# Optimization experiments

Hardware: AMD Instinct MI355X
Metric: run time of the kernel (lower is better)

## Reference

```python
import jax, jax.numpy as jnp
import numpy as np

C_IN = 256
A = 2086
H_BOARD, W_BOARD = 10, 9
S = H_BOARD * W_BOARD  # 90
E = 2                  # embed dim after 1x1 conv
NH = 2                 # num attention heads (head_dim = 1)
B = 4096
BN_EPS = 1e-5


def setup_inputs() -> dict:
    key = jax.random.key(0)
    ks = jax.random.split(key, 12)
    inp = {
        "x": jax.random.normal(ks[0], (B, C_IN, H_BOARD, W_BOARD), dtype=jnp.float32),
        # 1x1 conv, no bias: weight [out=2, in=256]
        "conv_w": jax.random.normal(ks[1], (E, C_IN), dtype=jnp.float32) * 0.05,
        # BatchNorm2d(2) params / running stats (inference-mode BN)
        "bn_gamma": jnp.ones((E,), dtype=jnp.float32),
        "bn_beta": jnp.zeros((E,), dtype=jnp.float32),
        "bn_mean": jax.random.normal(ks[2], (E,), dtype=jnp.float32) * 0.1,
        "bn_var": jax.random.uniform(ks[3], (E,), dtype=jnp.float32, minval=0.5, maxval=1.5),
        # MultiheadAttention packed in-proj: [3*E, E], bias [3*E]
        "in_proj_w": jax.random.normal(ks[4], (3 * E, E), dtype=jnp.float32) * 0.5,
        "in_proj_b": jax.random.normal(ks[5], (3 * E,), dtype=jnp.float32) * 0.05,
        "out_proj_w": jax.random.normal(ks[6], (E, E), dtype=jnp.float32) * 0.5,
        "out_proj_b": jax.random.normal(ks[7], (E,), dtype=jnp.float32) * 0.05,
        # Linear(2*90 -> 2086)
        "fc_w": jax.random.normal(ks[8], (A, E * S), dtype=jnp.float32) * 0.05,
        "fc_b": jax.random.normal(ks[9], (A,), dtype=jnp.float32) * 0.05,
    }
    return inp


def reference(x, conv_w, bn_gamma, bn_beta, bn_mean, bn_var,
              in_proj_w, in_proj_b, out_proj_w, out_proj_b, fc_w, fc_b):
    b = x.shape[0]
    # 1x1 conv (bias-free) == channel contraction: [b,256,h,w] -> [b,2,h,w]
    y = jnp.einsum('bchw,oc->bohw', x, conv_w)
    # BatchNorm2d (inference): (y - mean) / sqrt(var + eps) * gamma + beta
    scale = (bn_gamma * jax.lax.rsqrt(bn_var + BN_EPS))[None, :, None, None]
    shift = (bn_beta - bn_mean * bn_gamma * jax.lax.rsqrt(bn_var + BN_EPS))[None, :, None, None]
    y = y * scale + shift
    # [b,2,h,w] -> [b, S, 2]  (seq = board cells, feature = 2 channels)
    xf = y.reshape(b, E, S).transpose(0, 2, 1)
    # packed QKV projection
    qkv = xf @ in_proj_w.T + in_proj_b          # [b,S,3E]
    q, k, v = jnp.split(qkv, 3, axis=-1)        # each [b,S,E]
    hd = E // NH                                 # head_dim = 1
    def split_heads(t):
        return t.reshape(b, S, NH, hd).transpose(0, 2, 1, 3)  # [b,nh,S,hd]
    q, k, v = split_heads(q), split_heads(k), split_heads(v)
    scores = jnp.einsum('bhqd,bhkd->bhqk', q, k) / jnp.sqrt(jnp.float32(hd))
    attn = jax.nn.softmax(scores, axis=-1)      # [b,nh,S,S]
    o = jnp.einsum('bhqk,bhkd->bhqd', attn, v)  # [b,nh,S,hd]
    o = o.transpose(0, 2, 1, 3).reshape(b, S, E)
    o = o @ out_proj_w.T + out_proj_b           # [b,S,E]
    # [b,S,E] -> [b,E,S] -> [b, E*S], matching permute(0,2,1).view(b,-1)
    flat = o.transpose(0, 2, 1).reshape(b, E * S)
    logits = flat @ fc_w.T + fc_b               # [b, 2086]
    return logits
```

## Files before the change

### kernel.cpp

```cpp
#include <hip/hip_runtime.h>

#define C_IN    256
#define S_CELLS 90
#define A_OUT   2086
#define K_FC    180
#define B_BATCH 4096

__global__ __launch_bounds__(384) void front_kernel(
    const float* __restrict__ x,
    const float* __restrict__ conv_w,
    const float* __restrict__ bn_gamma,
    const float* __restrict__ bn_beta,
    const float* __restrict__ bn_mean,
    const float* __restrict__ bn_var,
    const float* __restrict__ ipw,
    const float* __restrict__ ipb,
    const float* __restrict__ opw,
    const float* __restrict__ opb,
    float* __restrict__ flat)
{
    __shared__ float4 kvpack[4][S_CELLS];

    const int sub = threadIdx.x / 96;
    const int s   = threadIdx.x % 96;
    const int b   = blockIdx.x * 4 + sub;

    float q0 = 0.f, q1 = 0.f;

    if (s < S_CELLS) {
        const float* xb = x + (size_t)b * (C_IN * S_CELLS) + s;
        float a0 = 0.f, a1 = 0.f;
        #pragma unroll 16
        for (int c = 0; c < C_IN; ++c) {
            float xv = xb[(size_t)c * S_CELLS];
            a0 = fmaf(conv_w[c], xv, a0);
            a1 = fmaf(conv_w[C_IN + c], xv, a1);
        }
        const float sc0 = bn_gamma[0] * rsqrtf(bn_var[0] + 1e-5f);
        const float sc1 = bn_gamma[1] * rsqrtf(bn_var[1] + 1e-5f);
        const float y0 = a0 * sc0 + (bn_beta[0] - bn_mean[0] * sc0);
        const float y1 = a1 * sc1 + (bn_beta[1] - bn_mean[1] * sc1);
        q0 = ipw[0] * y0 + ipw[1] * y1 + ipb[0];
        q1 = ipw[2] * y0 + ipw[3] * y1 + ipb[1];
        const float k0 = ipw[4] * y0 + ipw[5]  * y1 + ipb[2];
        const float k1 = ipw[6] * y0 + ipw[7]  * y1 + ipb[3];
        const float v0 = ipw[8] * y0 + ipw[9]  * y1 + ipb[4];
        const float v1 = ipw[10]* y0 + ipw[11] * y1 + ipb[5];
        kvpack[sub][s] = make_float4(k0, v0, k1, v1);
    }
    __syncthreads();
    if (s < S_CELLS) {
        float den0 = 0.f, num0 = 0.f, den1 = 0.f, num1 = 0.f;
        #pragma unroll 5
        for (int j = 0; j < S_CELLS; ++j) {
            const float4 kv = kvpack[sub][j];
            const float e0 = __expf(q0 * kv.x);
            const float e1 = __expf(q1 * kv.z);
            den0 += e0; num0 = fmaf(e0, kv.y, num0);
            den1 += e1; num1 = fmaf(e1, kv.w, num1);
        }
        const float o0 = num0 / den0;
        const float o1 = num1 / den1;
        const float r0 = opw[0] * o0 + opw[1] * o1 + opb[0];
        const float r1 = opw[2] * o0 + opw[3] * o1 + opb[1];
        flat[(size_t)b * K_FC + s]           = r0;
        flat[(size_t)b * K_FC + S_CELLS + s] = r1;
    }
}

#define BM 128
#define BN 128
#define BK 36
#define KV4 (BK / 4)

__global__ __launch_bounds__(256) void fc_kernel(
    const float* __restrict__ Af,
    const float* __restrict__ W,
    const float* __restrict__ bias,
    float* __restrict__ out)
{
    __shared__ __align__(16) float As[BK][BM + 4];
    __shared__ __align__(16) float Bs[BK][BN + 4];

    const int tid = threadIdx.x;
    const int tx  = tid & 15;
    const int ty  = tid >> 4;
    const int bm  = blockIdx.y * BM;
    const int bn  = blockIdx.x * BN;

    float acc[8][8] = {};

    for (int k0 = 0; k0 < K_FC; k0 += BK) {
        for (int q = tid; q < BM * KV4; q += 256) {
            const int m  = q / KV4;
            const int kv = q % KV4;
            const float4 v = *(const float4*)(Af + (size_t)(bm + m) * K_FC + k0 + kv * 4);
            const int kk = kv * 4;
            As[kk + 0][m] = v.x; As[kk + 1][m] = v.y;
            As[kk + 2][m] = v.z; As[kk + 3][m] = v.w;
        }
        for (int q = tid; q < BN * KV4; q += 256) {
            const int n  = q / KV4;
            const int kv = q % KV4;
            const int gn = bn + n;
            float4 v = make_float4(0.f, 0.f, 0.f, 0.f);
            if (gn < A_OUT)
                v = *(const float4*)(W + (size_t)gn * K_FC + k0 + kv * 4);
            const int kk = kv * 4;
            Bs[kk + 0][n] = v.x; Bs[kk + 1][n] = v.y;
            Bs[kk + 2][n] = v.z; Bs[kk + 3][n] = v.w;
        }
        __syncthreads();

        #pragma unroll 4
        for (int k = 0; k < BK; ++k) {
            float a[8], bb[8];
            const float4 a0 = *(const float4*)&As[k][ty * 8];
            const float4 a1 = *(const float4*)&As[k][ty * 8 + 4];
            const float4 b0 = *(const float4*)&Bs[k][tx * 8];
            const float4 b1 = *(const float4*)&Bs[k][tx * 8 + 4];
            a[0]=a0.x; a[1]=a0.y; a[2]=a0.z; a[3]=a0.w;
            a[4]=a1.x; a[5]=a1.y; a[6]=a1.z; a[7]=a1.w;
            bb[0]=b0.x; bb[1]=b0.y; bb[2]=b0.z; bb[3]=b0.w;
            bb[4]=b1.x; bb[5]=b1.y; bb[6]=b1.z; bb[7]=b1.w;
            #pragma unroll
            for (int i = 0; i < 8; ++i)
                #pragma unroll
                for (int j = 0; j < 8; ++j)
                    acc[i][j] = fmaf(a[i], bb[j], acc[i][j]);
        }
        __syncthreads();
    }

    #pragma unroll
    for (int i = 0; i < 8; ++i) {
        const int gm = bm + ty * 8 + i;
        #pragma unroll
        for (int p = 0; p < 4; ++p) {
            const int gn = bn + tx * 8 + p * 2;
            if (gn < A_OUT) {
                float2 v = make_float2(acc[i][p * 2]     + bias[gn],
                                       acc[i][p * 2 + 1] + bias[gn + 1]);
                *(float2*)(out + (size_t)gm * A_OUT + gn) = v;
            }
        }
    }
}

extern "C" void kernel_launch(void* const* d_in, const int* in_sizes, int n_in,
                              void* d_out, int out_size, void* d_ws, size_t ws_size,
                              hipStream_t stream) {
    const float* x        = (const float*)d_in[0];
    const float* conv_w   = (const float*)d_in[1];
    const float* bn_gamma = (const float*)d_in[2];
    const float* bn_beta  = (const float*)d_in[3];
    const float* bn_mean  = (const float*)d_in[4];
    const float* bn_var   = (const float*)d_in[5];
    const float* ipw      = (const float*)d_in[6];
    const float* ipb      = (const float*)d_in[7];
    const float* opw      = (const float*)d_in[8];
    const float* opb      = (const float*)d_in[9];
    const float* fc_w     = (const float*)d_in[10];
    const float* fc_b     = (const float*)d_in[11];
    float* out  = (float*)d_out;
    float* flat = (float*)d_ws;

    front_kernel<<<dim3(B_BATCH / 4), 384, 0, stream>>>(
        x, conv_w, bn_gamma, bn_beta, bn_mean, bn_var,
        ipw, ipb, opw, opb, flat);

    fc_kernel<<<dim3((A_OUT + BN - 1) / BN, B_BATCH / BM), 256, 0, stream>>>(
        flat, fc_w, fc_b, out);
}
```

Measured before the change: 593.7 us.

## Run FC layer on bf16 MFMA with padded bf16 activations and weights

The front kernel now writes its activations as bf16, zero-padded to K=192. A new kernel converts fc_w to padded bf16 on every call. The fp32 FMA GEMM is replaced with a bf16 MFMA 16x16x32 kernel that loads 64-wide K tiles into LDS. This moves the GEMM onto matrix cores and halves operand bytes, at the cost of bf16 precision loss and an extra weight-conversion launch.

```diff
diff --git a/kernel.cpp b/kernel.cpp
--- a/kernel.cpp
+++ b/kernel.cpp
@@ -4,7 +4,17 @@
 #define S_CELLS 90
 #define A_OUT   2086
 #define K_FC    180
+#define K_PAD   192
+#define N_PAD   2176
 #define B_BATCH 4096
+
+typedef __attribute__((ext_vector_type(8))) short short8;
+typedef __attribute__((ext_vector_type(4))) float floatx4;
+
+static __device__ __forceinline__ unsigned short f2bf(float f) {
+    unsigned u = __float_as_uint(f);
+    return (unsigned short)((u + 0x7FFFu + ((u >> 16) & 1u)) >> 16);
+}
 
 __global__ __launch_bounds__(384) void front_kernel(
     const float* __restrict__ x,
@@ -17,7 +27,7 @@
     const float* __restrict__ ipb,
     const float* __restrict__ opw,
     const float* __restrict__ opb,
-    float* __restrict__ flat)
+    unsigned short* __restrict__ Abf)
 {
     __shared__ float4 kvpack[4][S_CELLS];
 
@@ -63,86 +73,91 @@
         const float o1 = num1 / den1;
         const float r0 = opw[0] * o0 + opw[1] * o1 + opb[0];
         const float r1 = opw[2] * o0 + opw[3] * o1 + opb[1];
-        flat[(size_t)b * K_FC + s]           = r0;
-        flat[(size_t)b * K_FC + S_CELLS + s] = r1;
+        Abf[(size_t)b * K_PAD + s]           = f2bf(r0);
+        Abf[(size_t)b * K_PAD + S_CELLS + s] = f2bf(r1);
+    } else {
+        Abf[(size_t)b * K_PAD + 180 + (s - S_CELLS)] = 0;
+        Abf[(size_t)b * K_PAD + 186 + (s - S_CELLS)] = 0;
     }
+}
+
+__global__ __launch_bounds__(192) void wconv_kernel(
+    const float* __restrict__ W, unsigned short* __restrict__ Wbf)
+{
+    const int n = blockIdx.x;
+    const int k = threadIdx.x;
+    unsigned short v = 0;
+    if (n < A_OUT && k < K_FC) v = f2bf(W[(size_t)n * K_FC + k]);
+    Wbf[(size_t)n * K_PAD + k] = v;
 }
 
 #define BM 128
 #define BN 128
-#define BK 36
-#define KV4 (BK / 4)
+#define BK 64
+#define LDSROW 72
 
-__global__ __launch_bounds__(256) void fc_kernel(
-    const float* __restrict__ Af,
-    const float* __restrict__ W,
+__global__ __launch_bounds__(256) void fc_mfma_kernel(
+    const unsigned short* __restrict__ Abf,
+    const unsigned short* __restrict__ Wbf,
     const float* __restrict__ bias,
     float* __restrict__ out)
 {
-    __shared__ __align__(16) float As[BK][BM + 4];
-    __shared__ __align__(16) float Bs[BK][BN + 4];
+    __shared__ __align__(16) unsigned short As[BM * LDSROW];
+    __shared__ __align__(16) unsigned short Bs[BN * LDSROW];
 
-    const int tid = threadIdx.x;
-    const int tx  = tid & 15;
-    const int ty  = tid >> 4;
-    const int bm  = blockIdx.y * BM;
-    const int bn  = blockIdx.x * BN;
+    const int tid  = threadIdx.x;
+    const int lane = tid & 63;
+    const int wave = tid >> 6;
+    const int wy   = wave >> 1;
+    const int wx   = wave & 1;
+    const int lrow = lane & 15;
+    const int lk   = (lane >> 4) * 8;
+    const int bm   = blockIdx.y * BM;
+    const int bn   = blockIdx.x * BN;
 
-    float acc[8][8] = {};
+    floatx4 acc[4][4] = {};
 
-    for (int k0 = 0; k0 < K_FC; k0 += BK) {
-        for (int q = tid; q < BM * KV4; q += 256) {
-            const int m  = q / KV4;
-            const int kv = q % KV4;
-            const float4 v = *(const float4*)(Af + (size_t)(bm + m) * K_FC + k0 + kv * 4);
-            const int kk = kv * 4;
-            As[kk + 0][m] = v.x; As[kk + 1][m] = v.y;
-            As[kk + 2][m] = v.z; As[kk + 3][m] = v.w;
-        }
-        for (int q = tid; q < BN * KV4; q += 256) {
-            const int n  = q / KV4;
-            const int kv = q % KV4;
-            const int gn = bn + n;
-            float4 v = make_float4(0.f, 0.f, 0.f, 0.f);
-            if (gn < A_OUT)
-                v = *(const float4*)(W + (size_t)gn * K_FC + k0 + kv * 4);
-            const int kk = kv * 4;
-            Bs[kk + 0][n] = v.x; Bs[kk + 1][n] = v.y;
-            Bs[kk + 2][n] = v.z; Bs[kk + 3][n] = v.w;
+    for (int k0 = 0; k0 < K_PAD; k0 += BK) {
+        for (int q = tid; q < BM * 8; q += 256) {
+            const int m = q >> 3, c = q & 7;
+            *(int4*)&As[m * LDSROW + c * 8] =
+                *(const int4*)(Abf + (size_t)(bm + m) * K_PAD + k0 + c * 8);
+            *(int4*)&Bs[m * LDSROW + c * 8] =
+                *(const int4*)(Wbf + (size_t)(bn + m) * K_PAD + k0 + c * 8);
         }
         __syncthreads();
 
-        #pragma unroll 4
-        for (int k = 0; k < BK; ++k) {
-            float a[8], bb[8];
-            const float4 a0 = *(const float4*)&As[k][ty * 8];
-            const float4 a1 = *(const float4*)&As[k][ty * 8 + 4];
-            const float4 b0 = *(const float4*)&Bs[k][tx * 8];
-            const float4 b1 = *(const float4*)&Bs[k][tx * 8 + 4];
-            a[0]=a0.x; a[1]=a0.y; a[2]=a0.z; a[3]=a0.w;
-            a[4]=a1.x; a[5]=a1.y; a[6]=a1.z; a[7]=a1.w;
-            bb[0]=b0.x; bb[1]=b0.y; bb[2]=b0.z; bb[3]=b0.w;
-            bb[4]=b1.x; bb[5]=b1.y; bb[6]=b1.z; bb[7]=b1.w;
+        #pragma unroll
+        for (int ks = 0; ks < 2; ++ks) {
+            short8 af[4], bf[4];
             #pragma unroll
-            for (int i = 0; i < 8; ++i)
+            for (int t = 0; t < 4; ++t) {
+                af[t] = *(const short8*)&As[(wy * 64 + t * 16 + lrow) * LDSROW + ks * 32 + lk];
+                bf[t] = *(const short8*)&Bs[(wx * 64 + t * 16 + lrow) * LDSROW + ks * 32 + lk];
+            }
+            #pragma unroll
+            for (int mt = 0; mt < 4; ++mt)
                 #pragma unroll
-                for (int j = 0; j < 8; ++j)
-                    acc[i][j] = fmaf(a[i], bb[j], acc[i][j]);
+                for (int nt = 0; nt < 4; ++nt)
+                    acc[mt][nt] = __builtin_amdgcn_mfma_f32_16x16x32_bf16(
+                        af[mt], bf[nt], acc[mt][nt], 0, 0, 0);
         }
         __syncthreads();
     }
 
+    const int ccol = lane & 15;
+    const int crow = (lane >> 4) * 4;
     #pragma unroll
-    for (int i = 0; i < 8; ++i) {
-        const int gm = bm + ty * 8 + i;
+    for (int mt = 0; mt < 4; ++mt) {
         #pragma unroll
-        for (int p = 0; p < 4; ++p) {
-            const int gn = bn + tx * 8 + p * 2;
-            if (gn < A_OUT) {
-                float2 v = make_float2(acc[i][p * 2]     + bias[gn],
-                                       acc[i][p * 2 + 1] + bias[gn + 1]);
-                *(float2*)(out + (size_t)gm * A_OUT + gn) = v;
-            }
+        for (int nt = 0; nt < 4; ++nt) {
+            const int n_out = bn + wx * 64 + nt * 16 + ccol;
+            if (n_out >= A_OUT) continue;
+            const int m_base = bm + wy * 64 + mt * 16 + crow;
+            const float bv = bias[n_out];
+            #pragma unroll
+            for (int r = 0; r < 4; ++r)
+                out[(size_t)(m_base + r) * A_OUT + n_out] = acc[mt][nt][r] + bv;
         }
     }
 }
@@ -162,13 +177,17 @@
     const float* opb      = (const float*)d_in[9];
     const float* fc_w     = (const float*)d_in[10];
     const float* fc_b     = (const float*)d_in[11];
-    float* out  = (float*)d_out;
-    float* flat = (float*)d_ws;
+    float* out = (float*)d_out;
+
+    unsigned short* Abf = (unsigned short*)d_ws;
+    unsigned short* Wbf = (unsigned short*)((char*)d_ws + (size_t)B_BATCH * K_PAD * 2);
 
     front_kernel<<<dim3(B_BATCH / 4), 384, 0, stream>>>(
         x, conv_w, bn_gamma, bn_beta, bn_mean, bn_var,
-        ipw, ipb, opw, opb, flat);
+        ipw, ipb, opw, opb, Abf);
 
-    fc_kernel<<<dim3((A_OUT + BN - 1) / BN, B_BATCH / BM), 256, 0, stream>>>(
-        flat, fc_w, fc_b, out);
+    wconv_kernel<<<dim3(N_PAD), 192, 0, stream>>>(fc_w, Wbf);
+
+    fc_mfma_kernel<<<dim3(N_PAD / BN, B_BATCH / BM), 256, 0, stream>>>(
+        Abf, Wbf, fc_b, out);
 }
```

After: 545.7 us. 1.09x faster.
